# Kernel optimization log

Hardware: AMD Instinct MI355X
Metric: run time of the kernel (lower is better)

The kernel has to match this reference:

```python
import jax, jax.numpy as jnp
import numpy as np
import math

B, D_MODEL, SEQ_LEN, EMB_DIM, ORDER = 4, 1024, 4096, 5, 64


def setup_inputs() -> dict:
    key = jax.random.key(0)
    ks = jax.random.split(key, 12)
    L = SEQ_LEN
    # PositionalEmbedding: z = [t, Re(e^{-i f w}), Im(e^{-i f w})]
    t = jnp.linspace(0.0, 1.0, L)[None, :, None]                      # [1,L,1]
    bands = (EMB_DIM - 1) // 2
    t_rescaled = jnp.linspace(0.0, L - 1, L)[None, :, None]           # [1,L,1]
    w = 2 * math.pi * t_rescaled / L
    f = jnp.linspace(1e-4, bands - 1, bands)[None, None]              # [1,1,bands]
    zc = jnp.exp(-1j * f * w.astype(jnp.complex64))                   # [1,L,bands]
    z = jnp.concatenate([t, zc.real, zc.imag], axis=-1)               # [1,L,EMB_DIM]
    # ExponentialModulation deltas (fast_decay_pct=0.3, slow_decay_pct=1.5, target=0.01)
    max_decay = math.log(0.01) / 0.3
    min_decay = math.log(0.01) / 1.5
    deltas = jnp.linspace(min_decay, max_decay, D_MODEL)[None, None]  # [1,1,D]
    s = 0.1  # small init scale for MLP weights
    return {
        "x": jax.random.normal(ks[0], (B, D_MODEL, SEQ_LEN), jnp.float32),
        "L": SEQ_LEN,
        "z": z.astype(jnp.float32),
        "t": t.astype(jnp.float32),
        "deltas": deltas.astype(jnp.float32),
        "W1": jax.random.normal(ks[1], (ORDER, EMB_DIM), jnp.float32) * s,
        "b1": jax.random.normal(ks[2], (ORDER,), jnp.float32) * s,
        "freq": jnp.ones((1, ORDER), jnp.float32),  # Sin freq, w=1
        "W2": jax.random.normal(ks[3], (ORDER, ORDER), jnp.float32) * s,
        "b2": jax.random.normal(ks[4], (ORDER,), jnp.float32) * s,
        "W3": jax.random.normal(ks[5], (ORDER, ORDER), jnp.float32) * s,
        "b3": jax.random.normal(ks[6], (ORDER,), jnp.float32) * s,
        "W4": jax.random.normal(ks[7], (D_MODEL, ORDER), jnp.float32) * s,
        "bias": jax.random.normal(ks[8], (D_MODEL,), jnp.float32),
    }


def reference(x, L, z, t, deltas, W1, b1, freq, W2, b2, W3, b3, W4, bias):
    # --- implicit filter MLP: z [1,L,E] -> k [1,L,D] ---
    zL, tL = z[:, :L], t[:, :L]
    h = jnp.sin(freq * (jnp.einsum('ble,oe->blo', zL, W1) + b1))
    h = jnp.sin(freq * (jnp.einsum('blo,po->blp', h, W2) + b2))
    h = jnp.sin(freq * (jnp.einsum('blo,po->blp', h, W3) + b3))
    h = jnp.einsum('blo,do->bld', h, W4)                # [1,L,D], no bias
    # --- exponential modulation ---
    decay = jnp.exp(-tL * jnp.abs(deltas))              # [1,L,D]
    h = h * decay
    k = h[0].T                                          # [D, L] per-channel filters
    # --- FFT causal conv: irfft(rfft(u)*rfft(k)/n, norm='forward') == plain circular conv on 2L ---
    n = 2 * L
    u_f = jnp.fft.rfft(x, n=n)                          # [B,D,L+1] complex
    k_f = jnp.fft.rfft(k, n=n)                          # [D,L+1]
    y = jnp.fft.irfft(u_f * k_f, n=n)[..., :L]          # [B,D,L]
    out = y + x * bias[:, None]                         # D.unsqueeze(-1) bias term, gelu=False
    return out.astype(x.dtype)
```

## Files before the change

### kernel.cpp

```cpp
#include <hip/hip_runtime.h>
#include <math.h>


#define PAD(i) ((i) + ((i) >> 4))
#define TWO_PI 6.2831853071795864769f
#define C8 0.70710678118654752440f

typedef __attribute__((ext_vector_type(2))) float cplx;

static __device__ __forceinline__ cplx mkc(float x, float y) { cplx c; c.x = x; c.y = y; return c; }
static __device__ __forceinline__ cplx cswap(cplx v)  { return __builtin_shufflevector(v, v, 1, 0); }
static __device__ __forceinline__ cplx cimul(cplx v)  { return __builtin_shufflevector(v, -v, 3, 0); }
static __device__ __forceinline__ cplx cnimul(cplx v) { return __builtin_shufflevector(v, -v, 1, 2); }
static __device__ __forceinline__ cplx cconj(cplx v)  { return __builtin_shufflevector(v, -v, 0, 3); }
static __device__ __forceinline__ cplx splx(cplx v)   { return __builtin_shufflevector(v, v, 0, 0); }
static __device__ __forceinline__ cplx sply(cplx v)   { return __builtin_shufflevector(v, v, 1, 1); }

static __device__ __forceinline__ cplx cmulv(cplx a, cplx b) {
    return splx(b) * a + sply(b) * cimul(a);
}
static __device__ __forceinline__ cplx cmuljv(cplx a, cplx b) {
    return splx(a) * b + sply(a) * cnimul(b);
}

template <bool FWD>
__device__ __forceinline__ void dft8_pk(cplx v[8]) {
    const cplx w15 = FWD ? mkc(C8, -C8) : mkc(C8, C8);
    const cplx w37 = FWD ? mkc(-C8, -C8) : mkc(-C8, C8);
    cplx s0 = v[0] + v[4], s1 = v[0] - v[4];
    cplx s2 = v[2] + v[6], s3 = v[2] - v[6];
    cplx s4 = v[1] + v[5], s5 = v[1] - v[5];
    cplx s6 = v[3] + v[7], s7 = v[3] - v[7];
    cplx g0 = s0 + s2, g2 = s0 - s2;
    cplx g1 = FWD ? (s1 + cnimul(s3)) : (s1 + cimul(s3));
    cplx g3 = FWD ? (s1 + cimul(s3)) : (s1 + cnimul(s3));
    cplx g4 = s4 + s6, g6 = s4 - s6;
    cplx g5 = FWD ? (s5 + cnimul(s7)) : (s5 + cimul(s7));
    cplx g7 = FWD ? (s5 + cimul(s7)) : (s5 + cnimul(s7));
    v[0] = g0 + g4; v[4] = g0 - g4;
    cplx bt1 = cmulv(g5, w15);
    v[1] = g1 + bt1; v[5] = g1 - bt1;
    v[2] = FWD ? (g2 + cnimul(g6)) : (g2 + cimul(g6));
    v[6] = FWD ? (g2 + cimul(g6)) : (g2 + cnimul(g6));
    cplx bt3 = cmulv(g7, w37);
    v[3] = g3 + bt3; v[7] = g3 - bt3;
}

__device__ __forceinline__ void dft8_lo4_inv(cplx v[8]) {
    const cplx w15 = mkc(C8, C8), w37 = mkc(-C8, C8);
    cplx s0 = v[0] + v[4], s1 = v[0] - v[4];
    cplx s2 = v[2] + v[6], s3 = v[2] - v[6];
    cplx s4 = v[1] + v[5], s5 = v[1] - v[5];
    cplx s6 = v[3] + v[7], s7 = v[3] - v[7];
    cplx g0 = s0 + s2, g2 = s0 - s2;
    cplx g1 = s1 + cimul(s3), g3 = s1 + cnimul(s3);
    cplx g4 = s4 + s6, g6 = s4 - s6;
    cplx g5 = s5 + cimul(s7), g7 = s5 + cnimul(s7);
    v[0] = g0 + g4;
    v[1] = g1 + cmulv(g5, w15);
    v[2] = g2 + cimul(g6);
    v[3] = g3 + cmulv(g7, w37);
}

__device__ __forceinline__ void twiddle_powers(float ang, cplx w[8]) {
    float s, c;
    __sincosf(ang, &s, &c);
    w[1] = mkc(c, s);
    w[2] = cmulv(w[1], w[1]);
    w[3] = cmulv(w[2], w[1]);
    w[4] = cmulv(w[2], w[2]);
    w[5] = cmulv(w[4], w[1]);
    w[6] = cmulv(w[3], w[3]);
    w[7] = cmulv(w[4], w[3]);
}

template <int NS, bool FWD>
__device__ __forceinline__ void fft_pass_ip(cplx* __restrict__ buf, int j) {
    cplx* rp = buf + (j + (j >> 4));
    cplx v[8];
#pragma unroll
    for (int r = 0; r < 8; r++) v[r] = rp[544 * r];
    if (NS > 1) {
        int jm = j & (NS - 1);
        float ang = (FWD ? -1.0f : 1.0f) * (TWO_PI / (float)(NS * 8)) * (float)jm;
        cplx w[8];
        twiddle_powers(ang, w);
#pragma unroll
        for (int r = 1; r < 8; r++) v[r] = cmulv(v[r], w[r]);
    }
    dft8_pk<FWD>(v);
    __syncthreads();
    int base = ((j & ~(NS - 1)) << 3) + (j & (NS - 1));
    cplx* wp = buf + (base + (base >> 4));
#pragma unroll
    for (int r = 0; r < 8; r++) {
        const int off = (NS == 1) ? r
                      : (NS == 8) ? (8 * r + (r >> 1))
                      : (NS == 64) ? (68 * r)
                      : (544 * r);
        wp[off] = v[r];
    }
    __syncthreads();
}

__device__ __forceinline__ void fft_pass1_fwd_regs(cplx* __restrict__ buf, int j,
                                                   const cplx xv[4]) {
    const cplx w15 = mkc(C8, -C8), w37 = mkc(-C8, -C8);
    cplx a0 = xv[0] + xv[2], a2 = xv[0] - xv[2];
    cplx a1 = xv[0] + cnimul(xv[2]), a3 = xv[0] + cimul(xv[2]);
    cplx b0 = xv[1] + xv[3], b2 = xv[1] - xv[3];
    cplx b1 = xv[1] + cnimul(xv[3]), b3 = xv[1] + cimul(xv[3]);
    cplx v[8];
    v[0] = a0 + b0; v[4] = a0 - b0;
    cplx bt1 = cmulv(b1, w15);
    v[1] = a1 + bt1; v[5] = a1 - bt1;
    v[2] = a2 + cnimul(b2); v[6] = a2 + cimul(b2);
    cplx bt3 = cmulv(b3, w37);
    v[3] = a3 + bt3; v[7] = a3 - bt3;
    int b8 = 8 * j;
    cplx* wp = buf + (b8 + (b8 >> 4));
#pragma unroll
    for (int r = 0; r < 8; r++) wp[r] = v[r];
    __syncthreads();
}

__global__ __launch_bounds__(256) void mlp_kernel(
    const float* __restrict__ zin, const float* __restrict__ W1,
    const float* __restrict__ b1, const float* __restrict__ freq,
    const float* __restrict__ W2, const float* __restrict__ b2,
    const float* __restrict__ W3, const float* __restrict__ b3,
    float* __restrict__ h3T) {
    __shared__ float hs1[64][64];
    __shared__ float hs2[64][64];
    int tid = threadIdx.x;
    int l = tid & 63, w = tid >> 6;
    int lg = blockIdx.x * 64 + l;

    float zf[5];
#pragma unroll
    for (int e = 0; e < 5; e++) zf[e] = zin[lg * 5 + e];

#pragma unroll
    for (int i = 0; i < 16; i++) {
        int o = w * 16 + i;
        float a = b1[o];
#pragma unroll
        for (int e = 0; e < 5; e++) a += W1[o * 5 + e] * zf[e];
        hs1[o][l] = __sinf(freq[o] * a);
    }
    __syncthreads();

    float acc[16];
#pragma unroll
    for (int i = 0; i < 16; i++) acc[i] = b2[w * 16 + i];
#pragma unroll 8
    for (int o = 0; o < 64; o++) {
        float hv = hs1[o][l];
#pragma unroll
        for (int i = 0; i < 16; i++) acc[i] += W2[(w * 16 + i) * 64 + o] * hv;
    }
#pragma unroll
    for (int i = 0; i < 16; i++)
        hs2[w * 16 + i][l] = __sinf(freq[w * 16 + i] * acc[i]);
    __syncthreads();

#pragma unroll
    for (int i = 0; i < 16; i++) acc[i] = b3[w * 16 + i];
#pragma unroll 8
    for (int o = 0; o < 64; o++) {
        float hv = hs2[o][l];
#pragma unroll
        for (int i = 0; i < 16; i++) acc[i] += W3[(w * 16 + i) * 64 + o] * hv;
    }
#pragma unroll
    for (int i = 0; i < 16; i++)
        h3T[(size_t)(w * 16 + i) * 4096 + lg] = __sinf(freq[w * 16 + i] * acc[i]);
}

__global__ __launch_bounds__(256) void kgemm_kernel(
    const float* __restrict__ h3T, const float* __restrict__ W4,
    const float* __restrict__ tvec, const float* __restrict__ deltas,
    float* __restrict__ kout) {
    int lt = blockIdx.x & 3;
    int dt = blockIdx.x >> 2;
    int l0 = lt * 1024 + threadIdx.x * 4;
    float4 acc[16];
#pragma unroll
    for (int i = 0; i < 16; i++) acc[i] = make_float4(0.f, 0.f, 0.f, 0.f);
#pragma unroll 8
    for (int o = 0; o < 64; o++) {
        float4 h = *(const float4*)(h3T + (size_t)o * 4096 + l0);
#pragma unroll
        for (int i = 0; i < 16; i++) {
            float wv = W4[(size_t)(dt * 16 + i) * 64 + o];
            acc[i].x += wv * h.x; acc[i].y += wv * h.y;
            acc[i].z += wv * h.z; acc[i].w += wv * h.w;
        }
    }
    float4 tl = *(const float4*)(tvec + l0);
#pragma unroll
    for (int i = 0; i < 16; i++) {
        int d = dt * 16 + i;
        float da = fabsf(deltas[d]);
        float4 o;
        o.x = acc[i].x * __expf(-tl.x * da);
        o.y = acc[i].y * __expf(-tl.y * da);
        o.z = acc[i].z * __expf(-tl.z * da);
        o.w = acc[i].w * __expf(-tl.w * da);
        *(float4*)(kout + (size_t)d * 4096 + l0) = o;
    }
}

__global__ __launch_bounds__(512) void filter_fft_kernel(
    const float* __restrict__ kin, cplx* __restrict__ Kf) {
    __shared__ cplx buf[4352];
    int d = blockIdx.x, t = threadIdx.x;

    const cplx* k2 = (const cplx*)(kin + (size_t)d * 4096);
    cplx xv[4];
#pragma unroll
    for (int r = 0; r < 4; r++) xv[r] = k2[t + (r << 9)];
    fft_pass1_fwd_regs(buf, t, xv);
    fft_pass_ip<8, true>(buf, t);
    fft_pass_ip<64, true>(buf, t);
    fft_pass_ip<512, true>(buf, t);

    const float scale = 1.0f / 4096.0f;
    float sb, cb;
    __sincosf(-TWO_PI * (float)t * (1.0f / 8192.0f), &sb, &cb);
    cplx wk[4];
    wk[0] = mkc(cb, sb);
    wk[1] = cmulv(wk[0], mkc(0.92387953251128675613f, -0.38268343236508977173f));
    wk[2] = cmulv(wk[0], mkc(0.70710678118654752440f, -0.70710678118654752440f));
    wk[3] = cmulv(wk[0], mkc(0.38268343236508977173f, -0.92387953251128675613f));

    cplx* rb  = buf + (t + (t >> 4));
    cplx* qb2 = buf + (((4096 - t) + ((4096 - t) >> 4)) - 1632);
    cplx* KfRow = Kf + (size_t)d * 4104;
    cplx* kfp = KfRow + t;
    cplx* kfq = KfRow + (4096 - t);
#pragma unroll
    for (int i = 0; i < 4; i++) {
        if (t == 0 && i == 0) {
            cplx z0 = buf[0];
            KfRow[0]    = mkc((z0.x + z0.y) * scale, 0.f);
            KfRow[4096] = mkc((z0.x - z0.y) * scale, 0.f);
            cplx zm = buf[PAD(2048)];
            KfRow[2048] = mkc(zm.x * scale, -zm.y * scale);
        } else {
            cplx Zk = rb[544 * i];
            cplx Zq = qb2[544 * (3 - i)];
            cplx Fe = 0.5f * (Zk + cconj(Zq));
            cplx Fo = 0.5f * (cnimul(Zk) + cswap(Zq));
            cplx WFo = cmulv(wk[i], Fo);
            kfp[512 * i]  = scale * (Fe + WFo);
            kfq[-512 * i] = scale * cconj(Fe - WFo);
        }
    }
}

__global__ __launch_bounds__(512) void conv_kernel(
    const float* __restrict__ x, const cplx* __restrict__ Kf,
    const float* __restrict__ bias, float* __restrict__ out) {
    __shared__ cplx buf[4352];
    int rid = blockIdx.x;
    int d = rid & 1023;
    int t = threadIdx.x;

    const cplx* x2 = (const cplx*)(x + (size_t)rid * 4096);
    cplx xv[4];
#pragma unroll
    for (int r = 0; r < 4; r++) xv[r] = x2[t + (r << 9)];
    fft_pass1_fwd_regs(buf, t, xv);
    fft_pass_ip<8, true>(buf, t);
    fft_pass_ip<64, true>(buf, t);
    fft_pass_ip<512, true>(buf, t);

    float sb, cb;
    __sincosf(-TWO_PI * (float)t * (1.0f / 8192.0f), &sb, &cb);
    cplx wk[4];
    wk[0] = mkc(cb, sb);
    wk[1] = cmulv(wk[0], mkc(0.92387953251128675613f, -0.38268343236508977173f));
    wk[2] = cmulv(wk[0], mkc(0.70710678118654752440f, -0.70710678118654752440f));
    wk[3] = cmulv(wk[0], mkc(0.38268343236508977173f, -0.92387953251128675613f));

    cplx* rb  = buf + (t + (t >> 4));
    cplx* qb2 = buf + (((4096 - t) + ((4096 - t) >> 4)) - 1632);
    const cplx* KfRow = Kf + (size_t)d * 4104;
    const cplx* kfp = KfRow + t;
    const cplx* kfq = KfRow + (4096 - t);
#pragma unroll
    for (int i = 0; i < 4; i++) {
        if (t == 0 && i == 0) {
            cplx z0 = buf[0];
            float U0 = z0.x + z0.y;
            float UN = z0.x - z0.y;
            float Y0 = U0 * KfRow[0].x;
            float YN = UN * KfRow[4096].x;
            buf[0] = mkc(0.5f * (Y0 + YN), 0.5f * (Y0 - YN));
            cplx zm = buf[PAD(2048)];
            cplx Km = KfRow[2048];
            cplx Ym = mkc(zm.x * Km.x + zm.y * Km.y, zm.x * Km.y - zm.y * Km.x);
            buf[PAD(2048)] = mkc(Ym.x, -Ym.y);
        } else {
            cplx Zk = rb[544 * i];
            cplx Zq = qb2[544 * (3 - i)];
            cplx K1 = kfp[512 * i], K2 = kfq[-512 * i];
            cplx Fe = 0.5f * (Zk + cconj(Zq));
            cplx Fo = 0.5f * (cnimul(Zk) + cswap(Zq));
            cplx WFo = cmulv(wk[i], Fo);
            cplx U1 = Fe + WFo;
            cplx U2 = cconj(Fe - WFo);
            cplx Y1 = cmulv(U1, K1);
            cplx Y2 = cmulv(U2, K2);
            cplx FeY = 0.5f * (Y1 + cconj(Y2));
            cplx T   = 0.5f * (Y1 - cconj(Y2));
            cplx FoY = cmuljv(wk[i], T);
            rb[544 * i]        = FeY + cimul(FoY);
            qb2[544 * (3 - i)] = cconj(FeY - cimul(FoY));
        }
    }
    __syncthreads();

    fft_pass_ip<1, false>(buf, t);
    fft_pass_ip<8, false>(buf, t);
    fft_pass_ip<64, false>(buf, t);
    {
        cplx v[8];
#pragma unroll
        for (int r = 0; r < 8; r++) v[r] = rb[544 * r];
        float ang = (TWO_PI / 4096.0f) * (float)t;
        cplx w[8];
        twiddle_powers(ang, w);
#pragma unroll
        for (int r = 1; r < 8; r++) v[r] = cmulv(v[r], w[r]);
        dft8_lo4_inv(v);
        float bd = bias[d];
        cplx* o2 = (cplx*)(out + (size_t)rid * 4096);
#pragma unroll
        for (int r = 0; r < 4; r++) {
            o2[t + (r << 9)] = v[r] + bd * xv[r];
        }
    }
}

extern "C" void kernel_launch(void* const* d_in, const int* in_sizes, int n_in,
                              void* d_out, int out_size, void* d_ws, size_t ws_size,
                              hipStream_t stream) {
    const float* x      = (const float*)d_in[0];
    const float* zin    = (const float*)d_in[2];
    const float* tvec   = (const float*)d_in[3];
    const float* deltas = (const float*)d_in[4];
    const float* W1     = (const float*)d_in[5];
    const float* b1     = (const float*)d_in[6];
    const float* freq   = (const float*)d_in[7];
    const float* W2     = (const float*)d_in[8];
    const float* b2     = (const float*)d_in[9];
    const float* W3     = (const float*)d_in[10];
    const float* b3     = (const float*)d_in[11];
    const float* W4     = (const float*)d_in[12];
    const float* bias   = (const float*)d_in[13];
    float* out = (float*)d_out;

    float* h3T = (float*)d_ws;
    cplx*  Kf  = (cplx*)((char*)d_ws + (size_t)64 * 4096 * sizeof(float));
    float* kbuf = out + (size_t)3072 * 4096;

    mlp_kernel<<<64, 256, 0, stream>>>(zin, W1, b1, freq, W2, b2, W3, b3, h3T);
    kgemm_kernel<<<256, 256, 0, stream>>>(h3T, W4, tvec, deltas, kbuf);
    filter_fft_kernel<<<1024, 512, 0, stream>>>(kbuf, Kf);
    conv_kernel<<<4096, 512, 0, stream>>>(x, Kf, bias, out);
}
```

Before: 226.8 us.

## Use precomputed twiddle tables and fuse last FFT pass with spectral multiply

Replaces per-thread sincos plus twiddle-power chains with a global twiddle table that mlp_kernel fills, read through float4 loads. The last forward radix-8 pass now keeps its results in registers and feeds them straight into the real-FFT post-processing and spectral multiply. Half of the values are written to LDS for the partner thread, and the first inverse pass is done from registers. This cuts transcendental work and a couple of LDS round trips and barriers. In exchange it adds global/L2 table loads per pass, a special path for thread 0, and more register pressure.

```diff
diff --git a/kernel.cpp b/kernel.cpp
--- a/kernel.cpp
+++ b/kernel.cpp
@@ -62,31 +62,28 @@
     v[3] = g3 + cmulv(g7, w37);
 }
 
-__device__ __forceinline__ void twiddle_powers(float ang, cplx w[8]) {
-    float s, c;
-    __sincosf(ang, &s, &c);
-    w[1] = mkc(c, s);
-    w[2] = cmulv(w[1], w[1]);
-    w[3] = cmulv(w[2], w[1]);
-    w[4] = cmulv(w[2], w[2]);
-    w[5] = cmulv(w[4], w[1]);
-    w[6] = cmulv(w[3], w[3]);
-    w[7] = cmulv(w[4], w[3]);
+__device__ __forceinline__ void load_tw(const cplx* __restrict__ T, int row, cplx w[8]) {
+    const float4* tp = (const float4*)(T + ((size_t)row << 3));
+    float4 q0 = tp[0], q1 = tp[1], q2 = tp[2], q3 = tp[3];
+    w[1] = mkc(q0.z, q0.w);
+    w[2] = mkc(q1.x, q1.y); w[3] = mkc(q1.z, q1.w);
+    w[4] = mkc(q2.x, q2.y); w[5] = mkc(q2.z, q2.w);
+    w[6] = mkc(q3.x, q3.y); w[7] = mkc(q3.z, q3.w);
 }
 
 template <int NS, bool FWD>
-__device__ __forceinline__ void fft_pass_ip(cplx* __restrict__ buf, int j) {
+__device__ __forceinline__ void fft_pass_ip_tw(cplx* __restrict__ buf, int j,
+                                               const cplx* __restrict__ T) {
     cplx* rp = buf + (j + (j >> 4));
     cplx v[8];
 #pragma unroll
     for (int r = 0; r < 8; r++) v[r] = rp[544 * r];
-    if (NS > 1) {
-        int jm = j & (NS - 1);
-        float ang = (FWD ? -1.0f : 1.0f) * (TWO_PI / (float)(NS * 8)) * (float)jm;
+    {
+        int row = (j & (NS - 1)) * (512 / NS);
         cplx w[8];
-        twiddle_powers(ang, w);
-#pragma unroll
-        for (int r = 1; r < 8; r++) v[r] = cmulv(v[r], w[r]);
+        load_tw(T, row, w);
+#pragma unroll
+        for (int r = 1; r < 8; r++) v[r] = FWD ? cmulv(v[r], w[r]) : cmuljv(w[r], v[r]);
     }
     dft8_pk<FWD>(v);
     __syncthreads();
@@ -94,8 +91,7 @@
     cplx* wp = buf + (base + (base >> 4));
 #pragma unroll
     for (int r = 0; r < 8; r++) {
-        const int off = (NS == 1) ? r
-                      : (NS == 8) ? (8 * r + (r >> 1))
+        const int off = (NS == 8) ? (8 * r + (r >> 1))
                       : (NS == 64) ? (68 * r)
                       : (544 * r);
         wp[off] = v[r];
@@ -124,15 +120,34 @@
     __syncthreads();
 }
 
+#define W16_TABLE                                                             \
+    const cplx W16C1 = mkc(0.92387953251128675613f, -0.38268343236508977173f);\
+    const cplx W16C2 = mkc(0.70710678118654752440f, -0.70710678118654752440f);\
+    const cplx W16C3 = mkc(0.38268343236508977173f, -0.92387953251128675613f);
+
 __global__ __launch_bounds__(256) void mlp_kernel(
     const float* __restrict__ zin, const float* __restrict__ W1,
     const float* __restrict__ b1, const float* __restrict__ freq,
     const float* __restrict__ W2, const float* __restrict__ b2,
     const float* __restrict__ W3, const float* __restrict__ b3,
-    float* __restrict__ h3T) {
+    float* __restrict__ h3T, cplx* __restrict__ T, cplx* __restrict__ W0T) {
+    int tid = threadIdx.x;
+    int g = blockIdx.x * 256 + tid;
+    if (g < 4096) {
+        int m = g >> 3, r = g & 7;
+        int e = (m * r) & 4095;
+        float s, c;
+        __sincosf(-TWO_PI * (float)e * (1.0f / 4096.0f), &s, &c);
+        T[g] = mkc(c, s);
+    }
+    if (g < 512) {
+        float s, c;
+        __sincosf(-TWO_PI * (float)g * (1.0f / 8192.0f), &s, &c);
+        W0T[g] = mkc(c, s);
+    }
+
     __shared__ float hs1[64][64];
     __shared__ float hs2[64][64];
-    int tid = threadIdx.x;
     int l = tid & 63, w = tid >> 6;
     int lg = blockIdx.x * 64 + l;
 
@@ -212,7 +227,8 @@
 }
 
 __global__ __launch_bounds__(512) void filter_fft_kernel(
-    const float* __restrict__ kin, cplx* __restrict__ Kf) {
+    const float* __restrict__ kin, cplx* __restrict__ Kf,
+    const cplx* __restrict__ T, const cplx* __restrict__ W0T) {
     __shared__ cplx buf[4352];
     int d = blockIdx.x, t = threadIdx.x;
 
@@ -221,35 +237,58 @@
 #pragma unroll
     for (int r = 0; r < 4; r++) xv[r] = k2[t + (r << 9)];
     fft_pass1_fwd_regs(buf, t, xv);
-    fft_pass_ip<8, true>(buf, t);
-    fft_pass_ip<64, true>(buf, t);
-    fft_pass_ip<512, true>(buf, t);
+    fft_pass_ip_tw<8, true>(buf, t, T);
+    fft_pass_ip_tw<64, true>(buf, t, T);
+
+    cplx* rp = buf + (t + (t >> 4));
+    cplx zv[8];
+    {
+#pragma unroll
+        for (int r = 0; r < 8; r++) zv[r] = rp[544 * r];
+        cplx w[8];
+        load_tw(T, t, w);
+#pragma unroll
+        for (int r = 1; r < 8; r++) zv[r] = cmulv(zv[r], w[r]);
+        dft8_pk<true>(zv);
+    }
+#pragma unroll
+    for (int r = 4; r < 8; r++) rp[544 * r] = zv[r];
+    __syncthreads();
 
     const float scale = 1.0f / 4096.0f;
-    float sb, cb;
-    __sincosf(-TWO_PI * (float)t * (1.0f / 8192.0f), &sb, &cb);
+    cplx w0 = W0T[t];
+    W16_TABLE
     cplx wk[4];
-    wk[0] = mkc(cb, sb);
-    wk[1] = cmulv(wk[0], mkc(0.92387953251128675613f, -0.38268343236508977173f));
-    wk[2] = cmulv(wk[0], mkc(0.70710678118654752440f, -0.70710678118654752440f));
-    wk[3] = cmulv(wk[0], mkc(0.38268343236508977173f, -0.92387953251128675613f));
-
-    cplx* rb  = buf + (t + (t >> 4));
-    cplx* qb2 = buf + (((4096 - t) + ((4096 - t) >> 4)) - 1632);
+    wk[0] = w0;
+    wk[1] = cmulv(w0, W16C1);
+    wk[2] = cmulv(w0, W16C2);
+    wk[3] = cmulv(w0, W16C3);
     cplx* KfRow = Kf + (size_t)d * 4104;
-    cplx* kfp = KfRow + t;
-    cplx* kfq = KfRow + (4096 - t);
-#pragma unroll
-    for (int i = 0; i < 4; i++) {
-        if (t == 0 && i == 0) {
-            cplx z0 = buf[0];
-            KfRow[0]    = mkc((z0.x + z0.y) * scale, 0.f);
-            KfRow[4096] = mkc((z0.x - z0.y) * scale, 0.f);
-            cplx zm = buf[PAD(2048)];
-            KfRow[2048] = mkc(zm.x * scale, -zm.y * scale);
-        } else {
-            cplx Zk = rb[544 * i];
-            cplx Zq = qb2[544 * (3 - i)];
+    if (t == 0) {
+        cplx z0 = zv[0];
+        KfRow[0]    = mkc((z0.x + z0.y) * scale, 0.f);
+        KfRow[4096] = mkc((z0.x - z0.y) * scale, 0.f);
+        cplx zm = zv[4];
+        KfRow[2048] = mkc(zm.x * scale, -zm.y * scale);
+#pragma unroll
+        for (int i = 1; i < 4; i++) {
+            cplx Zk = zv[i];
+            cplx Zq = zv[8 - i];
+            cplx Fe = 0.5f * (Zk + cconj(Zq));
+            cplx Fo = 0.5f * (cnimul(Zk) + cswap(Zq));
+            cplx WFo = cmulv(wk[i], Fo);
+            KfRow[512 * i]        = scale * (Fe + WFo);
+            KfRow[4096 - 512 * i] = scale * cconj(Fe - WFo);
+        }
+    } else {
+        int p = 512 - t;
+        cplx* pb = buf + (p + (p >> 4));
+        cplx* kfp = KfRow + t;
+        cplx* kfq = KfRow + (4096 - t);
+#pragma unroll
+        for (int i = 0; i < 4; i++) {
+            cplx Zk = zv[i];
+            cplx Zq = pb[544 * (7 - i)];
             cplx Fe = 0.5f * (Zk + cconj(Zq));
             cplx Fo = 0.5f * (cnimul(Zk) + cswap(Zq));
             cplx WFo = cmulv(wk[i], Fo);
@@ -261,6 +300,7 @@
 
 __global__ __launch_bounds__(512) void conv_kernel(
     const float* __restrict__ x, const cplx* __restrict__ Kf,
+    const cplx* __restrict__ T, const cplx* __restrict__ W0T,
     const float* __restrict__ bias, float* __restrict__ out) {
     __shared__ cplx buf[4352];
     int rid = blockIdx.x;
@@ -272,74 +312,121 @@
 #pragma unroll
     for (int r = 0; r < 4; r++) xv[r] = x2[t + (r << 9)];
     fft_pass1_fwd_regs(buf, t, xv);
-    fft_pass_ip<8, true>(buf, t);
-    fft_pass_ip<64, true>(buf, t);
-    fft_pass_ip<512, true>(buf, t);
-
-    float sb, cb;
-    __sincosf(-TWO_PI * (float)t * (1.0f / 8192.0f), &sb, &cb);
-    cplx wk[4];
-    wk[0] = mkc(cb, sb);
-    wk[1] = cmulv(wk[0], mkc(0.92387953251128675613f, -0.38268343236508977173f));
-    wk[2] = cmulv(wk[0], mkc(0.70710678118654752440f, -0.70710678118654752440f));
-    wk[3] = cmulv(wk[0], mkc(0.38268343236508977173f, -0.92387953251128675613f));
-
-    cplx* rb  = buf + (t + (t >> 4));
-    cplx* qb2 = buf + (((4096 - t) + ((4096 - t) >> 4)) - 1632);
-    const cplx* KfRow = Kf + (size_t)d * 4104;
-    const cplx* kfp = KfRow + t;
-    const cplx* kfq = KfRow + (4096 - t);
-#pragma unroll
-    for (int i = 0; i < 4; i++) {
-        if (t == 0 && i == 0) {
-            cplx z0 = buf[0];
+    fft_pass_ip_tw<8, true>(buf, t, T);
+    fft_pass_ip_tw<64, true>(buf, t, T);
+
+    cplx* rp = buf + (t + (t >> 4));
+    cplx zv[8];
+    {
+#pragma unroll
+        for (int r = 0; r < 8; r++) zv[r] = rp[544 * r];
+        cplx w[8];
+        load_tw(T, t, w);
+#pragma unroll
+        for (int r = 1; r < 8; r++) zv[r] = cmulv(zv[r], w[r]);
+        dft8_pk<true>(zv);
+    }
+#pragma unroll
+    for (int r = 4; r < 8; r++) rp[544 * r] = zv[r];
+    __syncthreads();
+
+    cplx yl[4];
+    {
+        cplx w0 = W0T[t];
+        W16_TABLE
+        cplx wk[4];
+        wk[0] = w0;
+        wk[1] = cmulv(w0, W16C1);
+        wk[2] = cmulv(w0, W16C2);
+        wk[3] = cmulv(w0, W16C3);
+        const cplx* KfRow = Kf + (size_t)d * 4104;
+        if (t == 0) {
+            cplx z0 = zv[0];
             float U0 = z0.x + z0.y;
             float UN = z0.x - z0.y;
             float Y0 = U0 * KfRow[0].x;
             float YN = UN * KfRow[4096].x;
-            buf[0] = mkc(0.5f * (Y0 + YN), 0.5f * (Y0 - YN));
-            cplx zm = buf[PAD(2048)];
+            yl[0] = mkc(0.5f * (Y0 + YN), 0.5f * (Y0 - YN));
+            cplx zm = zv[4];
             cplx Km = KfRow[2048];
-            cplx Ym = mkc(zm.x * Km.x + zm.y * Km.y, zm.x * Km.y - zm.y * Km.x);
-            buf[PAD(2048)] = mkc(Ym.x, -Ym.y);
+            cplx Ym = cmuljv(zm, Km);
+            rp[544 * 4] = mkc(Ym.x, -Ym.y);
+#pragma unroll
+            for (int i = 1; i < 4; i++) {
+                cplx Zk = zv[i];
+                cplx Zq = zv[8 - i];
+                cplx K1 = KfRow[512 * i], K2 = KfRow[4096 - 512 * i];
+                cplx Fe = 0.5f * (Zk + cconj(Zq));
+                cplx Fo = 0.5f * (cnimul(Zk) + cswap(Zq));
+                cplx WFo = cmulv(wk[i], Fo);
+                cplx U1 = Fe + WFo;
+                cplx U2 = cconj(Fe - WFo);
+                cplx Y1 = cmulv(U1, K1);
+                cplx Y2 = cmulv(U2, K2);
+                cplx FeY = 0.5f * (Y1 + cconj(Y2));
+                cplx Tv  = 0.5f * (Y1 - cconj(Y2));
+                cplx FoY = cmuljv(wk[i], Tv);
+                yl[i] = FeY + cimul(FoY);
+                rp[544 * (8 - i)] = cconj(FeY - cimul(FoY));
+            }
         } else {
-            cplx Zk = rb[544 * i];
-            cplx Zq = qb2[544 * (3 - i)];
-            cplx K1 = kfp[512 * i], K2 = kfq[-512 * i];
-            cplx Fe = 0.5f * (Zk + cconj(Zq));
-            cplx Fo = 0.5f * (cnimul(Zk) + cswap(Zq));
-            cplx WFo = cmulv(wk[i], Fo);
-            cplx U1 = Fe + WFo;
-            cplx U2 = cconj(Fe - WFo);
-            cplx Y1 = cmulv(U1, K1);
-            cplx Y2 = cmulv(U2, K2);
-            cplx FeY = 0.5f * (Y1 + cconj(Y2));
-            cplx T   = 0.5f * (Y1 - cconj(Y2));
-            cplx FoY = cmuljv(wk[i], T);
-            rb[544 * i]        = FeY + cimul(FoY);
-            qb2[544 * (3 - i)] = cconj(FeY - cimul(FoY));
+            int p = 512 - t;
+            cplx* pb = buf + (p + (p >> 4));
+            const cplx* kfp = KfRow + t;
+            const cplx* kfq = KfRow + (4096 - t);
+#pragma unroll
+            for (int i = 0; i < 4; i++) {
+                cplx Zk = zv[i];
+                cplx Zq = pb[544 * (7 - i)];
+                cplx K1 = kfp[512 * i], K2 = kfq[-512 * i];
+                cplx Fe = 0.5f * (Zk + cconj(Zq));
+                cplx Fo = 0.5f * (cnimul(Zk) + cswap(Zq));
+                cplx WFo = cmulv(wk[i], Fo);
+                cplx U1 = Fe + WFo;
+                cplx U2 = cconj(Fe - WFo);
+                cplx Y1 = cmulv(U1, K1);
+                cplx Y2 = cmulv(U2, K2);
+                cplx FeY = 0.5f * (Y1 + cconj(Y2));
+                cplx Tv  = 0.5f * (Y1 - cconj(Y2));
+                cplx FoY = cmuljv(wk[i], Tv);
+                yl[i] = FeY + cimul(FoY);
+                pb[544 * (7 - i)] = cconj(FeY - cimul(FoY));
+            }
         }
     }
     __syncthreads();
 
-    fft_pass_ip<1, false>(buf, t);
-    fft_pass_ip<8, false>(buf, t);
-    fft_pass_ip<64, false>(buf, t);
-    {
-        cplx v[8];
-#pragma unroll
-        for (int r = 0; r < 8; r++) v[r] = rb[544 * r];
-        float ang = (TWO_PI / 4096.0f) * (float)t;
+    cplx v[8];
+#pragma unroll
+    for (int i = 0; i < 4; i++) v[i] = yl[i];
+#pragma unroll
+    for (int s = 0; s < 4; s++) v[4 + s] = rp[544 * (4 + s)];
+    __syncthreads();
+    dft8_pk<false>(v);
+    {
+        int b8 = 8 * t;
+        cplx* wp = buf + (b8 + (b8 >> 4));
+#pragma unroll
+        for (int r = 0; r < 8; r++) wp[r] = v[r];
+    }
+    __syncthreads();
+    fft_pass_ip_tw<8, false>(buf, t, T);
+    fft_pass_ip_tw<64, false>(buf, t, T);
+
+    {
+        cplx u[8];
+#pragma unroll
+        for (int r = 0; r < 8; r++) u[r] = rp[544 * r];
         cplx w[8];
-        twiddle_powers(ang, w);
-#pragma unroll
-        for (int r = 1; r < 8; r++) v[r] = cmulv(v[r], w[r]);
-        dft8_lo4_inv(v);
+        load_tw(T, t, w);
+#pragma unroll
+        for (int r = 1; r < 8; r++) u[r] = cmuljv(w[r], u[r]);
+        dft8_lo4_inv(u);
         float bd = bias[d];
         cplx* o2 = (cplx*)(out + (size_t)rid * 4096);
 #pragma unroll
         for (int r = 0; r < 4; r++) {
-            o2[t + (r << 9)] = v[r] + bd * xv[r];
+            o2[t + (r << 9)] = u[r] + bd * xv[r];
         }
     }
 }
@@ -363,11 +450,13 @@
     float* out = (float*)d_out;
 
     float* h3T = (float*)d_ws;
-    cplx*  Kf  = (cplx*)((char*)d_ws + (size_t)64 * 4096 * sizeof(float));
+    cplx*  Kf  = (cplx*)((char*)d_ws + (size_t)1048576);
+    cplx*  Tt  = (cplx*)((char*)d_ws + (size_t)1048576 + (size_t)33619968);
+    cplx*  W0T = (cplx*)((char*)d_ws + (size_t)1048576 + (size_t)33619968 + 32768);
     float* kbuf = out + (size_t)3072 * 4096;
 
-    mlp_kernel<<<64, 256, 0, stream>>>(zin, W1, b1, freq, W2, b2, W3, b3, h3T);
+    mlp_kernel<<<64, 256, 0, stream>>>(zin, W1, b1, freq, W2, b2, W3, b3, h3T, Tt, W0T);
     kgemm_kernel<<<256, 256, 0, stream>>>(h3T, W4, tvec, deltas, kbuf);
-    filter_fft_kernel<<<1024, 512, 0, stream>>>(kbuf, Kf);
-    conv_kernel<<<4096, 512, 0, stream>>>(x, Kf, bias, out);
-}
+    filter_fft_kernel<<<1024, 512, 0, stream>>>(kbuf, Kf, Tt, W0T);
+    conv_kernel<<<4096, 512, 0, stream>>>(x, Kf, Tt, W0T, bias, out);
+}
```

Result: slower. 277.6 us (+22.4%).
